# Performance work log

Measured on AMD Instinct MI355X. Metric: run time of the kernel, lower is better.

Reference implementation:

```python
import jax, jax.numpy as jnp
import numpy as np

T, B, I, H = 512, 64, 512, 512


def setup_inputs() -> dict:
    key = jax.random.key(0)
    ks = jax.random.split(key, 24)
    s = (1.0 / H) ** 0.5  # uniform_(-sqrt(1/hidden), sqrt(1/hidden))
    u = lambda k, shape: jax.random.uniform(k, shape, jnp.float32, -s, s)
    inp = {
        "x": jax.random.normal(ks[0], (T, B, I), jnp.float32),
        "h0": u(ks[1], (B, H)),
        "c0": u(ks[2], (B, H)),
    }
    j = 3
    for g in ("ii", "if", "ig", "io"):
        inp["W_" + g] = u(ks[j], (I, H)); j += 1
        inp["b_" + g] = u(ks[j], (H,)); j += 1
    for g in ("hi", "hf", "hg", "ho"):
        inp["W_" + g] = u(ks[j], (H, H)); j += 1
        inp["b_" + g] = u(ks[j], (H,)); j += 1
    return inp


def reference(x, h0, c0, W_ii, b_ii, W_if, b_if, W_ig, b_ig, W_io, b_io,
              W_hi, b_hi, W_hf, b_hf, W_hg, b_hg, W_ho, b_ho):
    # Concatenating per-gate weights is mathematically identical to the 8
    # separate matmuls + bias adds in the source cell.
    Wx = jnp.concatenate([W_ii, W_if, W_ig, W_io], axis=1)        # [I, 4H]
    Wh = jnp.concatenate([W_hi, W_hf, W_hg, W_ho], axis=1)        # [H, 4H]
    b = jnp.concatenate([b_ii + b_hi, b_if + b_hf, b_ig + b_hg, b_io + b_ho])
    # Precompute all input projections in one big GEMM: [T, B, 4H]
    xg = jnp.einsum('tbi,ih->tbh', x, Wx) + b

    def step(carry, xg_t):
        h, c = carry
        gates = xg_t + h @ Wh                                      # [B, 4H]
        i_g, f_g, g_g, o_g = jnp.split(gates, 4, axis=-1)
        i = jax.nn.sigmoid(i_g)
        f = jax.nn.sigmoid(f_g)
        g = jnp.tanh(g_g)
        o = jax.nn.sigmoid(o_g)
        c1 = f * c + i * g
        h1 = o * c1  # NOTE: source applies o * c_1 WITHOUT tanh(c_1)
        return (h1, c1), h1

    (hT, cT), out = jax.lax.scan(step, (h0, c0), xg)               # out: [T, B, H]
    return (out, hT, cT)
```

## Files before the change

kernel.cpp:

```cpp
#include <hip/hip_runtime.h>
#include <stdint.h>


typedef __attribute__((ext_vector_type(8))) short    short8;
typedef __attribute__((ext_vector_type(4))) float    f32x4;
typedef __attribute__((ext_vector_type(4))) unsigned u32x4;
typedef __attribute__((ext_vector_type(2))) unsigned u32x2;

#define XG_OFF    0ull
#define WBT_OFF   134217728ull
#define BIAS_OFF  136314880ull
#define HW_OFF    136323072ull

static __device__ __forceinline__ unsigned short f2bf(float f) {
  unsigned u = __float_as_uint(f);
  unsigned r = (u + 0x7FFFu + ((u >> 16) & 1u)) >> 16;
  return (unsigned short)r;
}
static __device__ __forceinline__ float bf2f(unsigned short u) {
  return __uint_as_float(((unsigned)u) << 16);
}
static __device__ __forceinline__ float sigmoidf_(float x) {
  return 1.0f / (1.0f + __expf(-x));
}
static __device__ __forceinline__ float tanhf_(float x) {
  return 1.0f - 2.0f / (__expf(2.0f * x) + 1.0f);
}

__global__ __launch_bounds__(256) void lstm_prep(
    const float* __restrict__ W_ii, const float* __restrict__ W_if,
    const float* __restrict__ W_ig, const float* __restrict__ W_io,
    const float* __restrict__ b_ii, const float* __restrict__ b_if,
    const float* __restrict__ b_ig, const float* __restrict__ b_io,
    const float* __restrict__ b_hi, const float* __restrict__ b_hf,
    const float* __restrict__ b_hg, const float* __restrict__ b_ho,
    const float* __restrict__ h0, unsigned char* ws)
{
  unsigned short*     WbT  = (unsigned short*)(ws + WBT_OFF);
  float*              bias = (float*)(ws + BIAS_OFF);
  unsigned long long* hw64 = (unsigned long long*)(ws + HW_OFF);

  const int bid = (int)blockIdx.x, tid = threadIdx.x;

  __shared__ float lds[32][33];

  const int g  = bid >> 8;
  const int tr = (bid >> 4) & 15;
  const int tc = bid & 15;
  const float* W = (g == 0) ? W_ii : (g == 1) ? W_if : (g == 2) ? W_ig : W_io;

  {
    const int kl = tid >> 3;
    const int c4 = (tid & 7) * 4;
    const float4 v = *reinterpret_cast<const float4*>(
        &W[(size_t)(tr * 32 + kl) * 512 + tc * 32 + c4]);
    lds[c4 + 0][kl] = v.x;
    lds[c4 + 1][kl] = v.y;
    lds[c4 + 2][kl] = v.z;
    lds[c4 + 3][kl] = v.w;
  }
  __syncthreads();
  {
    const int cl = tid >> 3;
    const int k4 = (tid & 7) * 4;
    const int gcol = g * 512 + tc * 32 + cl;
    uint2 p;
    p.x = (unsigned)f2bf(lds[cl][k4 + 0]) | ((unsigned)f2bf(lds[cl][k4 + 1]) << 16);
    p.y = (unsigned)f2bf(lds[cl][k4 + 2]) | ((unsigned)f2bf(lds[cl][k4 + 3]) << 16);
    *reinterpret_cast<uint2*>(&WbT[(size_t)gcol * 512 + tr * 32 + k4]) = p;
  }

  if (bid < 8) {
    int i = bid * 256 + tid;
    int gg = i >> 9, c = i & 511;
    const float* bi = (gg == 0) ? b_ii : (gg == 1) ? b_if : (gg == 2) ? b_ig : b_io;
    const float* bh = (gg == 0) ? b_hi : (gg == 1) ? b_hf : (gg == 2) ? b_hg : b_ho;
    bias[i] = bi[c] + bh[c];
  } else if (bid >= 64 && bid < 128) {
    int i = (bid - 64) * 256 + tid;
    int r = i >> 8, wc = i & 255;
    int gb = r >> 4, row = r & 15, wsl = wc >> 6, c = wc & 63;
    unsigned lo = f2bf(h0[(size_t)r * 512 + wc * 2]);
    unsigned hi = f2bf(h0[(size_t)r * 512 + wc * 2 + 1]);
    hw64[((size_t)(gb * 4 + wsl) * 16 + row) * 64 + c] =
        (unsigned long long)(lo | (hi << 16));
  } else if (bid >= 128 && bid < 192) {
    int i = (bid - 128) * 256 + tid;
    hw64[16384 + i] = 0xFFFFFFFF00000000ull;
  }
}

__global__ __launch_bounds__(256) void xproj_gemm(const float* __restrict__ x,
                                                  unsigned char* ws)
{
  const unsigned short* WbT  = (const unsigned short*)(ws + WBT_OFF);
  const float*          bias = (const float*)(ws + BIAS_OFF);
  unsigned short*       xg   = (unsigned short*)(ws + XG_OFF);

  __shared__ unsigned short As[128 * 64];
  __shared__ unsigned short Bs[128 * 64];

  const int bid  = (int)blockIdx.x;
  const int bidx = (bid & 7) * 512 + (bid >> 3);
  const int bm = bidx >> 4, bn = bidx & 15;
  const int row0 = bm * 128, col0 = bn * 128;

  const int tid = threadIdx.x, lane = tid & 63, w = tid >> 6;
  const int wr = w >> 1, wc = w & 1;

  f32x4 acc[4][4] = {};

  for (int k0 = 0; k0 < 512; k0 += 64) {
    __syncthreads();
#pragma unroll
    for (int u = 0; u < 8; ++u) {
      int idx = u * 256 + tid;
      int r = idx >> 4, quad = idx & 15;
      const float4 v = *reinterpret_cast<const float4*>(
          &x[(size_t)(row0 + r) * 512 + k0 + quad * 4]);
      uint2 p;
      p.x = (unsigned)f2bf(v.x) | ((unsigned)f2bf(v.y) << 16);
      p.y = (unsigned)f2bf(v.z) | ((unsigned)f2bf(v.w) << 16);
      *reinterpret_cast<uint2*>(&As[r * 64 + quad * 4]) = p;
    }
#pragma unroll
    for (int u = 0; u < 4; ++u) {
      int idx = u * 256 + tid;
      int cl = idx >> 3, ch = idx & 7;
      *reinterpret_cast<uint4*>(&Bs[cl * 64 + ch * 8]) =
          *reinterpret_cast<const uint4*>(&WbT[(size_t)(col0 + cl) * 512 + k0 + ch * 8]);
    }
    __syncthreads();
#pragma unroll
    for (int kk = 0; kk < 64; kk += 32) {
      short8 a[4], b[4];
#pragma unroll
      for (int m = 0; m < 4; ++m)
        a[m] = *reinterpret_cast<const short8*>(
            &As[(wr * 64 + m * 16 + (lane & 15)) * 64 + kk + (lane >> 4) * 8]);
#pragma unroll
      for (int n = 0; n < 4; ++n)
        b[n] = *reinterpret_cast<const short8*>(
            &Bs[(wc * 64 + n * 16 + (lane & 15)) * 64 + kk + (lane >> 4) * 8]);
#pragma unroll
      for (int m = 0; m < 4; ++m)
#pragma unroll
        for (int n = 0; n < 4; ++n)
          acc[m][n] = __builtin_amdgcn_mfma_f32_16x16x32_bf16(a[m], b[n], acc[m][n], 0, 0, 0);
    }
  }
#pragma unroll
  for (int m = 0; m < 4; ++m) {
    int rowtile = bm * 8 + wr * 4 + m;
#pragma unroll
    for (int n = 0; n < 4; ++n) {
      int coltile = bn * 8 + wc * 4 + n;
      float bv = bias[coltile * 16 + (lane & 15)];
      uint2 p;
      p.x = (unsigned)f2bf(acc[m][n][0] + bv) | ((unsigned)f2bf(acc[m][n][1] + bv) << 16);
      p.y = (unsigned)f2bf(acc[m][n][2] + bv) | ((unsigned)f2bf(acc[m][n][3] + bv) << 16);
      *reinterpret_cast<uint2*>(&xg[((size_t)rowtile * 128 + coltile) * 256 + lane * 4]) = p;
    }
  }
}

__global__ __launch_bounds__(256, 1) void lstm_rec(
    const float* __restrict__ Whi, const float* __restrict__ Whf,
    const float* __restrict__ Whg, const float* __restrict__ Who,
    const float* __restrict__ c0, unsigned char* ws, float* __restrict__ out)
{
  const int gb = (int)blockIdx.x & 3;
  const int gc = (int)blockIdx.x >> 2;
  const int tid = threadIdx.x, lane = tid & 63, w = tid >> 6;

  const unsigned short* xg = (const unsigned short*)(ws + XG_OFF);
  unsigned long long*   hw64 = (unsigned long long*)(ws + HW_OFF);

  __shared__ unsigned hdat[4][1024];
  __shared__ float glds[2][4][4][16][16];

  short8 bhi[4][4], blo[4][4];
  {
    const int colg = gc * 16 + (lane & 15);
    const int krow = (lane >> 4) * 8;
#pragma unroll
    for (int g = 0; g < 4; ++g) {
      const float* P = (g == 0) ? Whi : (g == 1) ? Whf : (g == 2) ? Whg : Who;
#pragma unroll
      for (int kkl = 0; kkl < 4; ++kkl) {
        short8 h8, l8;
#pragma unroll
        for (int i = 0; i < 8; ++i) {
          int k = w * 128 + kkl * 32 + krow + i;
          float wv = P[(size_t)k * 512 + colg];
          unsigned short hb = f2bf(wv);
          h8[i] = (short)hb;
          l8[i] = (short)f2bf(wv - bf2f(hb));
        }
        bhi[g][kkl] = h8; blo[g][kkl] = l8;
      }
    }
  }

  const int crow = tid >> 4, ccol = tid & 15;
  float c = c0[(size_t)(gb * 16 + crow) * 512 + gc * 16 + ccol];

  float* hT = out + 16777216;
  float* cT = out + 16777216 + 32768;
  const int e_ix = (crow >> 2) * 64 + ccol * 4 + (crow & 3);
  int bleft = 30000000;

  for (int t = 0; t < 512; ++t) {
    const size_t xb = (size_t)(t * 4 + gb) * 128 * 256;
    float xgi = bf2f(xg[xb + (size_t)(0 * 32 + gc) * 256 + e_ix]);
    float xgf = bf2f(xg[xb + (size_t)(1 * 32 + gc) * 256 + e_ix]);
    float xgg = bf2f(xg[xb + (size_t)(2 * 32 + gc) * 256 + e_ix]);
    float xgo = bf2f(xg[xb + (size_t)(3 * 32 + gc) * 256 + e_ix]);

    const int par = t & 1;
    const unsigned long long* blk =
        hw64 + (size_t)((par * 4 + gb) * 4 + w) * 1024;
    const unsigned tagw = (unsigned)t;

    u32x4 dv[8];
    const char* lbase = (const char*)blk + lane * 16;
    for (;;) {
#pragma unroll
      for (int i = 0; i < 8; ++i)
        asm volatile("global_load_dwordx4 %0, %1, off sc0 sc1"
                     : "=v"(dv[i]) : "v"(lbase + (size_t)i * 1024));
      asm volatile("s_waitcnt vmcnt(0)"
                   : "+v"(dv[0]), "+v"(dv[1]), "+v"(dv[2]), "+v"(dv[3]),
                     "+v"(dv[4]), "+v"(dv[5]), "+v"(dv[6]), "+v"(dv[7])
                   :: "memory");
      bool ok = true;
#pragma unroll
      for (int i = 0; i < 8; ++i)
        ok = ok && (dv[i][1] == tagw) && (dv[i][3] == tagw);
      if (__all(ok) || --bleft <= 0) break;
    }

#pragma unroll
    for (int i = 0; i < 8; ++i) {
      int k = i * 128 + lane * 2;
      int row = k >> 6;
      int sw = k ^ ((row & 7) << 2);
      u32x2 p2; p2[0] = dv[i][0]; p2[1] = dv[i][2];
      *reinterpret_cast<u32x2*>(&hdat[w][sw]) = p2;
    }
    asm volatile("s_waitcnt lgkmcnt(0)" ::: "memory");
    __builtin_amdgcn_sched_barrier(0);

    f32x4 acc[4] = {};
#pragma unroll
    for (int kkl = 0; kkl < 4; ++kkl) {
      int base = (lane & 15) * 64 + kkl * 16 + (lane >> 4) * 4;
      int sw = base ^ ((lane & 7) << 2);
      union { u32x4 v; short8 s; } fr;
      fr.v = *reinterpret_cast<const u32x4*>(&hdat[w][sw]);
#pragma unroll
      for (int g = 0; g < 4; ++g) {
        acc[g] = __builtin_amdgcn_mfma_f32_16x16x32_bf16(fr.s, bhi[g][kkl], acc[g], 0, 0, 0);
        acc[g] = __builtin_amdgcn_mfma_f32_16x16x32_bf16(fr.s, blo[g][kkl], acc[g], 0, 0, 0);
      }
    }
#pragma unroll
    for (int g = 0; g < 4; ++g)
#pragma unroll
      for (int j = 0; j < 4; ++j)
        glds[par][w][g][(lane >> 4) * 4 + j][lane & 15] = acc[g][j];
    __syncthreads();

    float gi = xgi, gf = xgf, gg = xgg, go = xgo;
#pragma unroll
    for (int ww = 0; ww < 4; ++ww) {
      gi += glds[par][ww][0][crow][ccol];
      gf += glds[par][ww][1][crow][ccol];
      gg += glds[par][ww][2][crow][ccol];
      go += glds[par][ww][3][crow][ccol];
    }
    float iv = sigmoidf_(gi), fv = sigmoidf_(gf), gv = tanhf_(gg), ov = sigmoidf_(go);
    c = fv * c + iv * gv;
    float h = ov * c;

    if (t != 511) {
      float h1 = __shfl_xor(h, 1);
      unsigned pack01 = (unsigned)f2bf(h) | ((unsigned)f2bf(h1) << 16);
      unsigned pack23 = (unsigned)__shfl_xor((int)pack01, 2);
      if ((ccol & 3) == 0) {
        u32x4 wp;
        wp[0] = pack01; wp[1] = (unsigned)(t + 1);
        wp[2] = pack23; wp[3] = (unsigned)(t + 1);
        unsigned long long* dst =
            hw64 + ((size_t)((((t + 1) & 1) * 4 + gb) * 4 + (gc >> 3)) * 16 + crow) * 64 +
            (gc & 7) * 8 + (ccol >> 1);
        asm volatile("global_store_dwordx4 %0, %1, off sc0 sc1"
                     :: "v"(dst), "v"(wp) : "memory");
      }
    }

    out[(size_t)t * 32768 + (size_t)(gb * 16 + crow) * 512 + gc * 16 + ccol] = h;
    if (t == 511) {
      hT[(size_t)(gb * 16 + crow) * 512 + gc * 16 + ccol] = h;
      cT[(size_t)(gb * 16 + crow) * 512 + gc * 16 + ccol] = c;
    }
  }
}

extern "C" void kernel_launch(void* const* d_in, const int* in_sizes, int n_in,
                              void* d_out, int out_size, void* d_ws, size_t ws_size,
                              hipStream_t stream)
{
  const float* x    = (const float*)d_in[0];
  const float* h0   = (const float*)d_in[1];
  const float* c0   = (const float*)d_in[2];
  const float* W_ii = (const float*)d_in[3];
  const float* b_ii = (const float*)d_in[4];
  const float* W_if = (const float*)d_in[5];
  const float* b_if = (const float*)d_in[6];
  const float* W_ig = (const float*)d_in[7];
  const float* b_ig = (const float*)d_in[8];
  const float* W_io = (const float*)d_in[9];
  const float* b_io = (const float*)d_in[10];
  const float* W_hi = (const float*)d_in[11];
  const float* b_hi = (const float*)d_in[12];
  const float* W_hf = (const float*)d_in[13];
  const float* b_hf = (const float*)d_in[14];
  const float* W_hg = (const float*)d_in[15];
  const float* b_hg = (const float*)d_in[16];
  const float* W_ho = (const float*)d_in[17];
  const float* b_ho = (const float*)d_in[18];
  unsigned char* ws = (unsigned char*)d_ws;
  float* out = (float*)d_out;

  hipLaunchKernelGGL(lstm_prep, dim3(1024), dim3(256), 0, stream,
                     W_ii, W_if, W_ig, W_io, b_ii, b_if, b_ig, b_io,
                     b_hi, b_hf, b_hg, b_ho, h0, ws);
  hipLaunchKernelGGL(xproj_gemm, dim3(4096), dim3(256), 0, stream, x, ws);
  hipLaunchKernelGGL(lstm_rec, dim3(128), dim3(256), 0, stream,
                     W_hi, W_hf, W_hg, W_ho, c0, ws, out);
}
```

Measured before the change: 1.118 ms.

## Fuse input-projection GEMM into recurrent kernel with per-row-block ready counters

Merges the input-projection GEMM and the recurrent LSTM kernel into one launch of 256 blocks. 128 producer blocks compute the projection tiles in time order and bump a per-row-block counter with release semantics. 128 recurrent blocks poll that counter before reading xg, so the serial recurrence can start while the GEMM is still running. The h-exchange store also shrinks from dwordx4 to dwordx2 per lane pair, and polling adds s_sleep. This relies on all 256 blocks being co-resident to avoid deadlock, and the GEMM now runs on only 128 CUs.

```diff
diff --git a/kernel.cpp b/kernel.cpp
--- a/kernel.cpp
+++ b/kernel.cpp
@@ -11,6 +11,7 @@
 #define WBT_OFF   134217728ull
 #define BIAS_OFF  136314880ull
 #define HW_OFF    136323072ull
+#define CNT_OFF   136585216ull
 
 static __device__ __forceinline__ unsigned short f2bf(float f) {
   unsigned u = __float_as_uint(f);
@@ -39,6 +40,7 @@
   unsigned short*     WbT  = (unsigned short*)(ws + WBT_OFF);
   float*              bias = (float*)(ws + BIAS_OFF);
   unsigned long long* hw64 = (unsigned long long*)(ws + HW_OFF);
+  unsigned*           cnt  = (unsigned*)(ws + CNT_OFF);
 
   const int bid = (int)blockIdx.x, tid = threadIdx.x;
 
@@ -87,97 +89,109 @@
   } else if (bid >= 128 && bid < 192) {
     int i = (bid - 128) * 256 + tid;
     hw64[16384 + i] = 0xFFFFFFFF00000000ull;
-  }
-}
-
-__global__ __launch_bounds__(256) void xproj_gemm(const float* __restrict__ x,
-                                                  unsigned char* ws)
-{
-  const unsigned short* WbT  = (const unsigned short*)(ws + WBT_OFF);
-  const float*          bias = (const float*)(ws + BIAS_OFF);
-  unsigned short*       xg   = (unsigned short*)(ws + XG_OFF);
-
-  __shared__ unsigned short As[128 * 64];
-  __shared__ unsigned short Bs[128 * 64];
-
-  const int bid  = (int)blockIdx.x;
-  const int bidx = (bid & 7) * 512 + (bid >> 3);
-  const int bm = bidx >> 4, bn = bidx & 15;
-  const int row0 = bm * 128, col0 = bn * 128;
-
-  const int tid = threadIdx.x, lane = tid & 63, w = tid >> 6;
-  const int wr = w >> 1, wc = w & 1;
-
-  f32x4 acc[4][4] = {};
-
-  for (int k0 = 0; k0 < 512; k0 += 64) {
-    __syncthreads();
-#pragma unroll
-    for (int u = 0; u < 8; ++u) {
-      int idx = u * 256 + tid;
-      int r = idx >> 4, quad = idx & 15;
-      const float4 v = *reinterpret_cast<const float4*>(
-          &x[(size_t)(row0 + r) * 512 + k0 + quad * 4]);
-      uint2 p;
-      p.x = (unsigned)f2bf(v.x) | ((unsigned)f2bf(v.y) << 16);
-      p.y = (unsigned)f2bf(v.z) | ((unsigned)f2bf(v.w) << 16);
-      *reinterpret_cast<uint2*>(&As[r * 64 + quad * 4]) = p;
-    }
-#pragma unroll
-    for (int u = 0; u < 4; ++u) {
-      int idx = u * 256 + tid;
-      int cl = idx >> 3, ch = idx & 7;
-      *reinterpret_cast<uint4*>(&Bs[cl * 64 + ch * 8]) =
-          *reinterpret_cast<const uint4*>(&WbT[(size_t)(col0 + cl) * 512 + k0 + ch * 8]);
-    }
-    __syncthreads();
-#pragma unroll
-    for (int kk = 0; kk < 64; kk += 32) {
-      short8 a[4], b[4];
-#pragma unroll
-      for (int m = 0; m < 4; ++m)
-        a[m] = *reinterpret_cast<const short8*>(
-            &As[(wr * 64 + m * 16 + (lane & 15)) * 64 + kk + (lane >> 4) * 8]);
-#pragma unroll
-      for (int n = 0; n < 4; ++n)
-        b[n] = *reinterpret_cast<const short8*>(
-            &Bs[(wc * 64 + n * 16 + (lane & 15)) * 64 + kk + (lane >> 4) * 8]);
-#pragma unroll
-      for (int m = 0; m < 4; ++m)
-#pragma unroll
-        for (int n = 0; n < 4; ++n)
-          acc[m][n] = __builtin_amdgcn_mfma_f32_16x16x32_bf16(a[m], b[n], acc[m][n], 0, 0, 0);
-    }
-  }
-#pragma unroll
-  for (int m = 0; m < 4; ++m) {
-    int rowtile = bm * 8 + wr * 4 + m;
-#pragma unroll
-    for (int n = 0; n < 4; ++n) {
-      int coltile = bn * 8 + wc * 4 + n;
-      float bv = bias[coltile * 16 + (lane & 15)];
-      uint2 p;
-      p.x = (unsigned)f2bf(acc[m][n][0] + bv) | ((unsigned)f2bf(acc[m][n][1] + bv) << 16);
-      p.y = (unsigned)f2bf(acc[m][n][2] + bv) | ((unsigned)f2bf(acc[m][n][3] + bv) << 16);
-      *reinterpret_cast<uint2*>(&xg[((size_t)rowtile * 128 + coltile) * 256 + lane * 4]) = p;
-    }
-  }
-}
-
-__global__ __launch_bounds__(256, 1) void lstm_rec(
+  } else if (bid == 192) {
+    cnt[tid] = 0u;
+  }
+}
+
+__global__ __launch_bounds__(256, 1) void lstm_fused(
+    const float* __restrict__ x,
     const float* __restrict__ Whi, const float* __restrict__ Whf,
     const float* __restrict__ Whg, const float* __restrict__ Who,
     const float* __restrict__ c0, unsigned char* ws, float* __restrict__ out)
 {
-  const int gb = (int)blockIdx.x & 3;
-  const int gc = (int)blockIdx.x >> 2;
+  const int bid = (int)blockIdx.x;
   const int tid = threadIdx.x, lane = tid & 63, w = tid >> 6;
 
-  const unsigned short* xg = (const unsigned short*)(ws + XG_OFF);
-  unsigned long long*   hw64 = (unsigned long long*)(ws + HW_OFF);
+  unsigned long long* hw64 = (unsigned long long*)(ws + HW_OFF);
+  unsigned*           cnt  = (unsigned*)(ws + CNT_OFF);
 
   __shared__ unsigned hdat[4][1024];
   __shared__ float glds[2][4][4][16][16];
+  __shared__ unsigned short As[128 * 64];
+  __shared__ unsigned short Bs[128 * 64];
+
+  if (bid < 128) {
+    const unsigned short* WbT  = (const unsigned short*)(ws + WBT_OFF);
+    const float*          bias = (const float*)(ws + BIAS_OFF);
+    unsigned short*       xg   = (unsigned short*)(ws + XG_OFF);
+    const int j  = bid;
+    const int wr = w >> 1, wc = w & 1;
+
+    for (int s = 0; s < 32; ++s) {
+      const int bm = 8 * s + (j >> 4);
+      const int bn = j & 15;
+      const int row0 = bm * 128, col0 = bn * 128;
+
+      f32x4 acc[4][4] = {};
+      for (int k0 = 0; k0 < 512; k0 += 64) {
+        __syncthreads();
+#pragma unroll
+        for (int u = 0; u < 8; ++u) {
+          int idx = u * 256 + tid;
+          int r = idx >> 4, quad = idx & 15;
+          const float4 v = *reinterpret_cast<const float4*>(
+              &x[(size_t)(row0 + r) * 512 + k0 + quad * 4]);
+          uint2 p;
+          p.x = (unsigned)f2bf(v.x) | ((unsigned)f2bf(v.y) << 16);
+          p.y = (unsigned)f2bf(v.z) | ((unsigned)f2bf(v.w) << 16);
+          *reinterpret_cast<uint2*>(&As[r * 64 + quad * 4]) = p;
+        }
+#pragma unroll
+        for (int u = 0; u < 4; ++u) {
+          int idx = u * 256 + tid;
+          int cl = idx >> 3, ch = idx & 7;
+          *reinterpret_cast<uint4*>(&Bs[cl * 64 + ch * 8]) =
+              *reinterpret_cast<const uint4*>(&WbT[(size_t)(col0 + cl) * 512 + k0 + ch * 8]);
+        }
+        __syncthreads();
+#pragma unroll
+        for (int kk = 0; kk < 64; kk += 32) {
+          short8 a[4], b[4];
+#pragma unroll
+          for (int m = 0; m < 4; ++m)
+            a[m] = *reinterpret_cast<const short8*>(
+                &As[(wr * 64 + m * 16 + (lane & 15)) * 64 + kk + (lane >> 4) * 8]);
+#pragma unroll
+          for (int n = 0; n < 4; ++n)
+            b[n] = *reinterpret_cast<const short8*>(
+                &Bs[(wc * 64 + n * 16 + (lane & 15)) * 64 + kk + (lane >> 4) * 8]);
+#pragma unroll
+          for (int m = 0; m < 4; ++m)
+#pragma unroll
+            for (int n = 0; n < 4; ++n)
+              acc[m][n] = __builtin_amdgcn_mfma_f32_16x16x32_bf16(a[m], b[n], acc[m][n], 0, 0, 0);
+        }
+      }
+#pragma unroll
+      for (int m = 0; m < 4; ++m) {
+        int rowtile = bm * 8 + wr * 4 + m;
+#pragma unroll
+        for (int n = 0; n < 4; ++n) {
+          int coltile = bn * 8 + wc * 4 + n;
+          float bv = bias[coltile * 16 + (lane & 15)];
+          u32x2 p;
+          p[0] = (unsigned)f2bf(acc[m][n][0] + bv) | ((unsigned)f2bf(acc[m][n][1] + bv) << 16);
+          p[1] = (unsigned)f2bf(acc[m][n][2] + bv) | ((unsigned)f2bf(acc[m][n][3] + bv) << 16);
+          unsigned short* dst = &xg[((size_t)rowtile * 128 + coltile) * 256 + lane * 4];
+          asm volatile("global_store_dwordx2 %0, %1, off sc0 sc1"
+                       :: "v"(dst), "v"(p) : "memory");
+        }
+      }
+      asm volatile("s_waitcnt vmcnt(0)" ::: "memory");
+      __syncthreads();
+      if (tid == 0)
+        __hip_atomic_fetch_add(&cnt[bm], 1u, __ATOMIC_RELEASE,
+                               __HIP_MEMORY_SCOPE_AGENT);
+    }
+    return;
+  }
+
+  const int rbid = bid - 128;
+  const int gb = rbid & 3;
+  const int gc = rbid >> 2;
+
+  const unsigned short* xg = (const unsigned short*)(ws + XG_OFF);
 
   short8 bhi[4][4], blo[4][4];
   {
@@ -211,16 +225,25 @@
   int bleft = 30000000;
 
   for (int t = 0; t < 512; ++t) {
+    const int par = t & 1;
+    const unsigned tagw = (unsigned)t;
+    const int bmn = (t * 4 + gb) >> 3;
+
+    unsigned cntv = __hip_atomic_load(&cnt[bmn], __ATOMIC_RELAXED,
+                                      __HIP_MEMORY_SCOPE_AGENT);
     const size_t xb = (size_t)(t * 4 + gb) * 128 * 256;
-    float xgi = bf2f(xg[xb + (size_t)(0 * 32 + gc) * 256 + e_ix]);
-    float xgf = bf2f(xg[xb + (size_t)(1 * 32 + gc) * 256 + e_ix]);
-    float xgg = bf2f(xg[xb + (size_t)(2 * 32 + gc) * 256 + e_ix]);
-    float xgo = bf2f(xg[xb + (size_t)(3 * 32 + gc) * 256 + e_ix]);
-
-    const int par = t & 1;
+    const unsigned short* xp0 = &xg[xb + (size_t)(0 * 32 + gc) * 256 + e_ix];
+    const unsigned short* xp1 = &xg[xb + (size_t)(1 * 32 + gc) * 256 + e_ix];
+    const unsigned short* xp2 = &xg[xb + (size_t)(2 * 32 + gc) * 256 + e_ix];
+    const unsigned short* xp3 = &xg[xb + (size_t)(3 * 32 + gc) * 256 + e_ix];
+    unsigned xu0, xu1, xu2, xu3;
+    asm volatile("global_load_ushort %0, %1, off sc0 sc1" : "=v"(xu0) : "v"(xp0));
+    asm volatile("global_load_ushort %0, %1, off sc0 sc1" : "=v"(xu1) : "v"(xp1));
+    asm volatile("global_load_ushort %0, %1, off sc0 sc1" : "=v"(xu2) : "v"(xp2));
+    asm volatile("global_load_ushort %0, %1, off sc0 sc1" : "=v"(xu3) : "v"(xp3));
+
     const unsigned long long* blk =
         hw64 + (size_t)((par * 4 + gb) * 4 + w) * 1024;
-    const unsigned tagw = (unsigned)t;
 
     u32x4 dv[8];
     const char* lbase = (const char*)blk + lane * 16;
@@ -238,7 +261,25 @@
       for (int i = 0; i < 8; ++i)
         ok = ok && (dv[i][1] == tagw) && (dv[i][3] == tagw);
       if (__all(ok) || --bleft <= 0) break;
-    }
+      __builtin_amdgcn_s_sleep(1);
+    }
+
+    if (cntv < 16u) {
+      do {
+        cntv = __hip_atomic_load(&cnt[bmn], __ATOMIC_RELAXED,
+                                 __HIP_MEMORY_SCOPE_AGENT);
+      } while (cntv < 16u && --bleft > 0);
+      asm volatile("global_load_ushort %0, %1, off sc0 sc1" : "=v"(xu0) : "v"(xp0));
+      asm volatile("global_load_ushort %0, %1, off sc0 sc1" : "=v"(xu1) : "v"(xp1));
+      asm volatile("global_load_ushort %0, %1, off sc0 sc1" : "=v"(xu2) : "v"(xp2));
+      asm volatile("global_load_ushort %0, %1, off sc0 sc1" : "=v"(xu3) : "v"(xp3));
+      asm volatile("s_waitcnt vmcnt(0)"
+                   : "+v"(xu0), "+v"(xu1), "+v"(xu2), "+v"(xu3) :: "memory");
+    }
+    float xgi = bf2f((unsigned short)xu0);
+    float xgf = bf2f((unsigned short)xu1);
+    float xgg = bf2f((unsigned short)xu2);
+    float xgo = bf2f((unsigned short)xu3);
 
 #pragma unroll
     for (int i = 0; i < 8; ++i) {
@@ -284,17 +325,14 @@
     float h = ov * c;
 
     if (t != 511) {
-      float h1 = __shfl_xor(h, 1);
-      unsigned pack01 = (unsigned)f2bf(h) | ((unsigned)f2bf(h1) << 16);
-      unsigned pack23 = (unsigned)__shfl_xor((int)pack01, 2);
-      if ((ccol & 3) == 0) {
-        u32x4 wp;
-        wp[0] = pack01; wp[1] = (unsigned)(t + 1);
-        wp[2] = pack23; wp[3] = (unsigned)(t + 1);
+      float hp = __shfl_xor(h, 1);
+      if ((ccol & 1) == 0) {
+        unsigned data = (unsigned)f2bf(h) | ((unsigned)f2bf(hp) << 16);
+        u32x2 wp; wp[0] = data; wp[1] = (unsigned)(t + 1);
         unsigned long long* dst =
             hw64 + ((size_t)((((t + 1) & 1) * 4 + gb) * 4 + (gc >> 3)) * 16 + crow) * 64 +
             (gc & 7) * 8 + (ccol >> 1);
-        asm volatile("global_store_dwordx4 %0, %1, off sc0 sc1"
+        asm volatile("global_store_dwordx2 %0, %1, off sc0 sc1"
                      :: "v"(dst), "v"(wp) : "memory");
       }
     }
@@ -336,7 +374,6 @@
   hipLaunchKernelGGL(lstm_prep, dim3(1024), dim3(256), 0, stream,
                      W_ii, W_if, W_ig, W_io, b_ii, b_if, b_ig, b_io,
                      b_hi, b_hf, b_hg, b_ho, h0, ws);
-  hipLaunchKernelGGL(xproj_gemm, dim3(4096), dim3(256), 0, stream, x, ws);
-  hipLaunchKernelGGL(lstm_rec, dim3(128), dim3(256), 0, stream,
-                     W_hi, W_hf, W_hg, W_ho, c0, ws, out);
-}
+  hipLaunchKernelGGL(lstm_fused, dim3(256), dim3(256), 0, stream,
+                     x, W_hi, W_hf, W_hg, W_ho, c0, ws, out);
+}
```

Measured after the change: 1.172 ms. 4.9% more time.
